# Optimization experiments

Hardware: AMD Instinct MI355X
Metric: run time of the kernel (lower is better)

Reference implementation:

```python
import jax, jax.numpy as jnp
import numpy as np

EPS = 1e-6
B, T, E, H = 2, 512, 1024, 256
NUM_BLOCK = 12


def normalize(x):
    # RMS-style normalization over the feature dim (no learned affine)
    return x * jax.lax.rsqrt(jnp.mean(x * x, axis=-1, keepdims=True) + EPS)


def bar_quadratic_causal(a, b):
    # y_i = (1/i) * sum_{j<=i} relu(a_i + b_j)   (causal prefix mean of pairwise relation)
    # a, b: [B, T, H]
    Tn = a.shape[1]
    pair = jax.nn.relu(a[:, :, None, :] + b[:, None, :, :])  # [B, T(i), T(j), H]
    mask = jnp.tril(jnp.ones((Tn, Tn), dtype=a.dtype))        # causal j<=i
    s = jnp.einsum('bijh,ij->bih', pair, mask)
    counts = jnp.arange(1, Tn + 1, dtype=a.dtype)[None, :, None]
    return s / counts


def setup_inputs() -> dict:
    key = jax.random.key(0)
    k0, k1, k2, k3 = jax.random.split(key, 4)
    x = jax.random.normal(k0, (B, T, E), dtype=jnp.float32)
    w1 = jax.random.normal(k1, (E, H), dtype=jnp.float32) * 0.02
    b1 = jnp.zeros((H,), dtype=jnp.float32)
    w2 = jax.random.normal(k2, (E, H), dtype=jnp.float32) * 0.02
    b2 = jnp.zeros((H,), dtype=jnp.float32)
    w3 = jax.random.normal(k3, (H, E), dtype=jnp.float32) * (0.02 / np.sqrt(NUM_BLOCK))
    b3 = jnp.zeros((E,), dtype=jnp.float32)
    return {"x": x, "w1": w1, "b1": b1, "w2": w2, "b2": b2, "w3": w3, "b3": b3}


def reference(x, w1, b1, w2, b2, w3, b3):
    r = normalize(x)
    a = r @ w1 + b1
    b = r @ w2 + b2
    # PreNorm == 'approx': normalize a and b separately
    a = normalize(a)
    b = normalize(b)
    r = bar_quadratic_causal(a, b)
    # PostNorm == 'yes'
    r = normalize(r)
    r = r @ w3 + b3
    return x + r
```

## Files before the change

kernel.cpp:

```cpp
#include <hip/hip_runtime.h>

#define EPSF 1e-6f
#define Bsz 2
#define Tn  512
#define En  1024
#define Hn  256
#define Mtot (Bsz * Tn)
typedef unsigned short us_t;
typedef unsigned int   u32_t;

typedef __attribute__((ext_vector_type(8))) __fp16 f16x8;
typedef __attribute__((ext_vector_type(2))) __fp16 h2_t;
typedef __attribute__((ext_vector_type(8))) short  short8;
typedef __attribute__((ext_vector_type(4))) float  f32x4;
#define MFMA16(a, b, c) __builtin_amdgcn_mfma_f32_16x16x32_f16((a), (b), (c), 0, 0, 0)

__device__ __forceinline__ us_t f2h(float f) {
  __fp16 h = (__fp16)f;
  return __builtin_bit_cast(us_t, h);
}
__device__ __forceinline__ float h2f(us_t u) {
  return (float)__builtin_bit_cast(__fp16, u);
}
__device__ __forceinline__ uint2 pack4h(float a, float b, float c, float d) {
  uint2 r;
  r.x = (u32_t)f2h(a) | ((u32_t)f2h(b) << 16);
  r.y = (u32_t)f2h(c) | ((u32_t)f2h(d) << 16);
  return r;
}
__device__ __forceinline__ float block_reduce_sum_256(float v, float* smem) {
  #pragma unroll
  for (int off = 32; off > 0; off >>= 1) v += __shfl_down(v, off, 64);
  const int wave = threadIdx.x >> 6;
  if ((threadIdx.x & 63) == 0) smem[wave] = v;
  __syncthreads();
  float s = smem[0] + smem[1] + smem[2] + smem[3];
  __syncthreads();
  return s;
}

__global__ __launch_bounds__(256) void k_prep(
    const float* __restrict__ x,
    const float* __restrict__ w1, const float* __restrict__ w2,
    const float* __restrict__ w3,
    us_t* __restrict__ xb, float* __restrict__ rs,
    us_t* __restrict__ w1t, us_t* __restrict__ w2t, us_t* __restrict__ w3t)
{
  const int b = blockIdx.x, t = threadIdx.x;

  if (b < 256) {
    const int wid = t >> 6, lane = t & 63;
    const int q   = b >> 3;
    const int mt  = (b & 7) + 8 * (q & 7);
    const int row = 16 * mt + 4 * (q >> 3) + wid;
    const float4* xp = (const float4*)(x + (size_t)row * En);
    float4 v[4];
    #pragma unroll
    for (int i = 0; i < 4; ++i) v[i] = xp[lane + 64 * i];
    float ss = 0.f;
    #pragma unroll
    for (int i = 0; i < 4; ++i)
      ss += v[i].x*v[i].x + v[i].y*v[i].y + v[i].z*v[i].z + v[i].w*v[i].w;
    #pragma unroll
    for (int off = 32; off > 0; off >>= 1) ss += __shfl_xor(ss, off, 64);
    if (lane == 0) rs[row] = rsqrtf(ss * (1.0f / En) + EPSF);
    uint2* xo = (uint2*)(xb + (size_t)row * En);
    #pragma unroll
    for (int i = 0; i < 4; ++i)
      xo[lane + 64 * i] = pack4h(v[i].x, v[i].y, v[i].z, v[i].w);
    return;
  }

  __shared__ float ts[32][33];
  const int i = b - 256;
  const float* src; us_t* dst; int R, C, tr, tc;
  if (i < 256)      { src = w1; dst = w1t; R = 1024; C = 256;  tr = i >> 3;  tc = i & 7; }
  else if (i < 512) { int k = i - 256; src = w2; dst = w2t; R = 1024; C = 256; tr = k >> 3; tc = k & 7; }
  else              { int k = i - 512; src = w3; dst = w3t; R = 256; C = 1024; tr = k >> 5; tc = k & 31; }

  const int r = t >> 3, c4 = (t & 7) * 4;
  float4 v = *(const float4*)(src + (size_t)(tr * 32 + r) * C + tc * 32 + c4);
  ts[r][c4 + 0] = v.x; ts[r][c4 + 1] = v.y; ts[r][c4 + 2] = v.z; ts[r][c4 + 3] = v.w;
  __syncthreads();
  float o0 = ts[c4 + 0][r], o1 = ts[c4 + 1][r], o2 = ts[c4 + 2][r], o3 = ts[c4 + 3][r];
  *(uint2*)(dst + (size_t)(tc * 32 + r) * R + tr * 32 + c4) = pack4h(o0, o1, o2, o3);
}

__global__ __launch_bounds__(256, 4) void k_gemm(
    const us_t* __restrict__ xb,
    const us_t* __restrict__ w1t, const us_t* __restrict__ w2t,
    float* __restrict__ Praw)
{
  const int blk = blockIdx.x;
  const int mt = blk & 63, nt = blk >> 6;
  const int m0 = mt * 16, n0 = nt * 32;
  const int wid = threadIdx.x >> 6, lane = threadIdx.x & 63;
  const int lg = lane >> 4, lr = lane & 15;
  const int k0 = wid * 256;

  const us_t* ap = xb + (size_t)(m0 + lr) * En + k0 + lg * 8;
  const us_t* bbase = (n0 < Hn) ? (w1t + (size_t)n0 * En)
                                : (w2t + (size_t)(n0 - Hn) * En);
  const us_t* bp0 = bbase + (size_t)lr * En + k0 + lg * 8;
  const us_t* bp1 = bp0 + (size_t)16 * En;

  f16x8 a[8], wf0[8], wf1[8];
  #pragma unroll
  for (int s = 0; s < 8; ++s) a[s]   = *(const f16x8*)(ap  + s * 32);
  #pragma unroll
  for (int s = 0; s < 8; ++s) wf0[s] = *(const f16x8*)(bp0 + s * 32);
  #pragma unroll
  for (int s = 0; s < 8; ++s) wf1[s] = *(const f16x8*)(bp1 + s * 32);

  f32x4 acc0 = {0.f,0.f,0.f,0.f}, acc1 = acc0;
  #pragma unroll
  for (int s = 0; s < 8; ++s) {
    acc0 = MFMA16(a[s], wf0[s], acc0);
    acc1 = MFMA16(a[s], wf1[s], acc1);
  }

  __shared__ float cmb[4][16][32];
  #pragma unroll
  for (int i = 0; i < 4; ++i) {
    cmb[wid][lg * 4 + i][lr]      = acc0[i];
    cmb[wid][lg * 4 + i][16 + lr] = acc1[i];
  }
  __syncthreads();

  #pragma unroll
  for (int e = 0; e < 2; ++e) {
    const int idx = threadIdx.x + e * 256;
    const int row = idx >> 5, col = idx & 31;
    float s = cmb[0][row][col] + cmb[1][row][col]
            + cmb[2][row][col] + cmb[3][row][col];
    Praw[(size_t)(m0 + row) * 512 + n0 + col] = s;
  }
}

__global__ __launch_bounds__(256) void k_norm(
    const float* __restrict__ Praw, const float* __restrict__ rs,
    const float* __restrict__ b2, us_t* __restrict__ BmT)
{
  const int blk = blockIdx.x, t = threadIdx.x;
  const int wid = t >> 6, lane = t & 63;
  const int h0 = lane * 4;

  __shared__ us_t ls[4][256];
  const int mt = blk & 63, sub = blk >> 6;
  const int r0 = 16 * mt + 4 * sub;
  const int r  = r0 + wid;

  float4 d = *(const float4*)(Praw + (size_t)r * 512 + Hn + h0);
  const float s0 = rs[r];
  float4 bv = *(const float4*)(b2 + h0);
  float vx = d.x * s0 + bv.x, vy = d.y * s0 + bv.y;
  float vz = d.z * s0 + bv.z, vw = d.w * s0 + bv.w;

  float ss = vx*vx + vy*vy + vz*vz + vw*vw;
  #pragma unroll
  for (int o2 = 32; o2 > 0; o2 >>= 1) ss += __shfl_xor(ss, o2, 64);
  const float sc = rsqrtf(ss * (1.0f / Hn) + EPSF);

  *(uint2*)&ls[wid][h0] = pack4h(vx*sc, vy*sc, vz*sc, vw*sc);
  __syncthreads();

  const int h = t;
  u32_t w0  = (u32_t)ls[0][h] | ((u32_t)ls[1][h] << 16);
  u32_t w1v = (u32_t)ls[2][h] | ((u32_t)ls[3][h] << 16);
  const int bb   = r0 >> 9;
  const int tcol = r0 & 511;
  *(uint2*)(BmT + (size_t)bb * Hn * Tn + (size_t)h * Tn + tcol) = make_uint2(w0, w1v);
}

#define JCHB 32
__global__ __launch_bounds__(256) void k_bar(
    const float* __restrict__ Praw, const float* __restrict__ rs,
    const float* __restrict__ b1,
    const us_t* __restrict__ BmT, us_t* __restrict__ Yb)
{
  __shared__ float red[4];
  const int raw = blockIdx.x;
  const int sel = (raw < 256) ? raw : (511 - raw);
  const int bb  = raw >> 8;
  const int i0  = sel * 2;
  const int h   = threadIdx.x;
  const int rg  = bb * Tn + i0;
  const size_t baseY = (size_t)bb * Tn * Hn;
  const us_t* __restrict__ bt = BmT + (size_t)bb * Hn * Tn + (size_t)h * Tn;

  const float b1h = b1[h];
  float v0 = fmaf(Praw[(size_t)rg * 512 + h],       rs[rg],     b1h);
  float v1 = fmaf(Praw[(size_t)(rg + 1) * 512 + h], rs[rg + 1], b1h);
  float ss0 = block_reduce_sum_256(v0 * v0, red);
  float ss1 = block_reduce_sum_256(v1 * v1, red);
  const float av0 = v0 * rsqrtf(ss0 * (1.0f / Hn) + EPSF);
  const float av1 = v1 * rsqrtf(ss1 * (1.0f / Hn) + EPSF);

  const __fp16 a0h = (__fp16)av0;
  const __fp16 a1h = (__fp16)av1;
  h2_t z2;  z2[0]  = (__fp16)0.f; z2[1]  = (__fp16)0.f;
  h2_t a02; a02[0] = a0h;         a02[1] = a0h;
  h2_t a12; a12[0] = a1h;         a12[1] = a1h;
  float sum0 = 0.f, sum1 = 0.f;

  const int nfull = i0 & ~(JCHB - 1);
  short8 c0[4], c1[4];

  #define LOADC(dst, jj) { _Pragma("unroll") \
    for (int q = 0; q < 4; ++q) dst[q] = *(const short8*)(bt + (jj) + q * 8); }
  #define PROCP(buf) { _Pragma("unroll") \
    for (int q = 0; q < 4; ++q) { \
      const h2_t* ph = (const h2_t*)&buf[q]; \
      h2_t p0 = z2, p1 = z2; \
      _Pragma("unroll") \
      for (int w2i = 0; w2i < 4; ++w2i) { \
        h2_t bv2 = ph[w2i]; \
        p0 += __builtin_elementwise_max(a02 + bv2, z2); \
        p1 += __builtin_elementwise_max(a12 + bv2, z2); \
      } \
      sum0 += (float)p0[0] + (float)p0[1]; \
      sum1 += (float)p1[0] + (float)p1[1]; } }

  if (nfull > 0) {
    LOADC(c0, 0);
    int j = 0;
    while (true) {
      const bool m1 = (j + JCHB     < nfull);
      const bool m2 = (j + 2 * JCHB < nfull);
      if (m1) LOADC(c1, j + JCHB);
      PROCP(c0);
      j += JCHB;
      if (!m1) break;
      if (m2) LOADC(c0, j + JCHB);
      PROCP(c1);
      j += JCHB;
      if (!m2) break;
    }
  }
  {
    short8 ct[4];
    LOADC(ct, nfull);
    const int lim = i0 - nfull;
    #pragma unroll
    for (int q = 0; q < 4; ++q)
      #pragma unroll
      for (int e = 0; e < 8; ++e) {
        const int jl = q * 8 + e;
        float bv = h2f((us_t)ct[q][e]);
        sum0 += (jl <= lim)     ? fmaxf((float)a0h + bv, 0.f) : 0.f;
        sum1 += (jl <= lim + 1) ? fmaxf((float)a1h + bv, 0.f) : 0.f;
      }
  }
  #undef LOADC
  #undef PROCP

  {
    float ss = block_reduce_sum_256(sum0 * sum0, red);
    float c  = (float)(i0 + 1);
    float sc = rsqrtf(ss * (1.0f / Hn) + EPSF * c * c);
    Yb[baseY + (size_t)i0 * Hn + h] = f2h(sum0 * sc);
  }
  {
    float ss = block_reduce_sum_256(sum1 * sum1, red);
    float c  = (float)(i0 + 2);
    float sc = rsqrtf(ss * (1.0f / Hn) + EPSF * c * c);
    Yb[baseY + (size_t)(i0 + 1) * Hn + h] = f2h(sum1 * sc);
  }
}

__global__ __launch_bounds__(256, 4) void k_out(
    const us_t* __restrict__ Yb, const us_t* __restrict__ w3t,
    const float* __restrict__ x, const float* __restrict__ b3,
    float* __restrict__ out)
{
  const int wid = threadIdx.x >> 6, lane = threadIdx.x & 63;
  const int wg = blockIdx.x * 4 + wid;
  const int nt = wg & 63, mt = wg >> 6;
  const int m0 = mt * 16, n0 = nt * 16;
  const int lg = lane >> 4, lr = lane & 15;

  const us_t* ap = Yb  + (size_t)(m0 + lr) * Hn + lg * 8;
  const us_t* bp = w3t + (size_t)(n0 + lr) * Hn + lg * 8;

  f16x8 a[8], b[8];
  #pragma unroll
  for (int s = 0; s < 8; ++s) a[s] = *(const f16x8*)(ap + s * 32);
  #pragma unroll
  for (int s = 0; s < 8; ++s) b[s] = *(const f16x8*)(bp + s * 32);

  f32x4 acc = {0.f,0.f,0.f,0.f};
  #pragma unroll
  for (int s = 0; s < 8; ++s) acc = MFMA16(a[s], b[s], acc);

  const int row = m0 + lg * 4;
  const int c = n0 + lr;
  const float bv = b3[c];
  #pragma unroll
  for (int i = 0; i < 4; ++i) {
    const size_t o = (size_t)(row + i) * En + c;
    out[o] = x[o] + acc[i] + bv;
  }
}

extern "C" void kernel_launch(void* const* d_in, const int* in_sizes, int n_in,
                              void* d_out, int out_size, void* d_ws, size_t ws_size,
                              hipStream_t stream) {
  const float* x  = (const float*)d_in[0];
  const float* w1 = (const float*)d_in[1];
  const float* b1 = (const float*)d_in[2];
  const float* w2 = (const float*)d_in[3];
  const float* b2 = (const float*)d_in[4];
  const float* w3 = (const float*)d_in[5];
  const float* b3 = (const float*)d_in[6];
  float* out = (float*)d_out;

  char* q = (char*)d_ws;
  float* Praw = (float*)q;  q += (size_t)Mtot * 512 * 4;
  us_t* xb    = (us_t*)q;   q += (size_t)Mtot * En * 2;
  us_t* w1t   = (us_t*)q;   q += (size_t)Hn * En * 2;
  us_t* w2t   = (us_t*)q;   q += (size_t)Hn * En * 2;
  us_t* w3t   = (us_t*)q;   q += (size_t)En * Hn * 2;
  us_t* BmT   = (us_t*)q;   q += (size_t)Mtot * Hn * 2;
  us_t* Yb    = (us_t*)q;   q += (size_t)Mtot * Hn * 2;
  float* rs   = (float*)q;  q += (size_t)Mtot * 4;

  k_prep<<<1024, 256, 0, stream>>>(x, w1, w2, w3, xb, rs, w1t, w2t, w3t);
  k_gemm<<<1024, 256, 0, stream>>>(xb, w1t, w2t, Praw);
  k_norm<<<256,  256, 0, stream>>>(Praw, rs, b2, BmT);
  k_bar <<<512,  256, 0, stream>>>(Praw, rs, b1, BmT, Yb);
  k_out <<<1024, 256, 0, stream>>>(Yb, w3t, x, b3, out);
}
```

Baseline: 47.06 us.

## Stage GEMM weight tiles through LDS via direct global-to-LDS loads

The projection GEMM now copies each wave's weight slice into swizzled shared memory with global_load_lds, instead of loading it into registers with per-lane vector loads. Each block now computes a 16-wide N tile rather than 32 wide, and the grid grows from 1024 to 2048 blocks. The aim is more coalesced weight fetches, lower register pressure and more parallelism. In exchange, the activation rows are loaded twice as often, and each block adds an extra barrier plus LDS round trips.

```diff
diff --git a/kernel.cpp b/kernel.cpp
--- a/kernel.cpp
+++ b/kernel.cpp
@@ -15,6 +15,10 @@
 typedef __attribute__((ext_vector_type(4))) float  f32x4;
 #define MFMA16(a, b, c) __builtin_amdgcn_mfma_f32_16x16x32_f16((a), (b), (c), 0, 0, 0)
 
+#define GLOAD_LDS16(g, l) __builtin_amdgcn_global_load_lds( \
+  (const __attribute__((address_space(1))) unsigned int*)(g), \
+  (__attribute__((address_space(3))) unsigned int*)(l), 16, 0, 0)
+
 __device__ __forceinline__ us_t f2h(float f) {
   __fp16 h = (__fp16)f;
   return __builtin_bit_cast(us_t, h);
@@ -91,50 +95,51 @@
     const us_t* __restrict__ w1t, const us_t* __restrict__ w2t,
     float* __restrict__ Praw)
 {
+  __shared__ us_t Bs[4][16][256];
+  __shared__ float cmb[4][16][16];
+
   const int blk = blockIdx.x;
   const int mt = blk & 63, nt = blk >> 6;
-  const int m0 = mt * 16, n0 = nt * 32;
-  const int wid = threadIdx.x >> 6, lane = threadIdx.x & 63;
+  const int m0 = mt * 16, n0 = nt * 16;
+  const int t = threadIdx.x;
+  const int wid = t >> 6, lane = t & 63;
   const int lg = lane >> 4, lr = lane & 15;
   const int k0 = wid * 256;
 
   const us_t* ap = xb + (size_t)(m0 + lr) * En + k0 + lg * 8;
+  f16x8 a[8];
+  #pragma unroll
+  for (int s = 0; s < 8; ++s) a[s] = *(const f16x8*)(ap + s * 32);
+
   const us_t* bbase = (n0 < Hn) ? (w1t + (size_t)n0 * En)
                                 : (w2t + (size_t)(n0 - Hn) * En);
-  const us_t* bp0 = bbase + (size_t)lr * En + k0 + lg * 8;
-  const us_t* bp1 = bp0 + (size_t)16 * En;
-
-  f16x8 a[8], wf0[8], wf1[8];
-  #pragma unroll
-  for (int s = 0; s < 8; ++s) a[s]   = *(const f16x8*)(ap  + s * 32);
-  #pragma unroll
-  for (int s = 0; s < 8; ++s) wf0[s] = *(const f16x8*)(bp0 + s * 32);
-  #pragma unroll
-  for (int s = 0; s < 8; ++s) wf1[s] = *(const f16x8*)(bp1 + s * 32);
-
-  f32x4 acc0 = {0.f,0.f,0.f,0.f}, acc1 = acc0;
+  #pragma unroll
+  for (int i = 0; i < 8; ++i) {
+    const int r   = 2 * i + (lane >> 5);
+    const int c2b = ((lane & 31) * 16) ^ ((r & 7) << 4);
+    const us_t* g = bbase + (size_t)r * En + k0 + (c2b >> 1);
+    GLOAD_LDS16(g, &Bs[wid][2 * i][0]);
+  }
+  __syncthreads();
+
+  f32x4 acc = {0.f,0.f,0.f,0.f};
+  const us_t* bs = &Bs[wid][0][0];
   #pragma unroll
   for (int s = 0; s < 8; ++s) {
-    acc0 = MFMA16(a[s], wf0[s], acc0);
-    acc1 = MFMA16(a[s], wf1[s], acc1);
-  }
-
-  __shared__ float cmb[4][16][32];
-  #pragma unroll
-  for (int i = 0; i < 4; ++i) {
-    cmb[wid][lg * 4 + i][lr]      = acc0[i];
-    cmb[wid][lg * 4 + i][16 + lr] = acc1[i];
-  }
-  __syncthreads();
-
-  #pragma unroll
-  for (int e = 0; e < 2; ++e) {
-    const int idx = threadIdx.x + e * 256;
-    const int row = idx >> 5, col = idx & 31;
-    float s = cmb[0][row][col] + cmb[1][row][col]
-            + cmb[2][row][col] + cmb[3][row][col];
-    Praw[(size_t)(m0 + row) * 512 + n0 + col] = s;
-  }
+    const int c2 = (lg * 16 + s * 64) ^ ((lr & 7) << 4);
+    f16x8 b = *(const f16x8*)(bs + lr * 256 + (c2 >> 1));
+    acc = MFMA16(a[s], b, acc);
+  }
+
+  #pragma unroll
+  for (int i = 0; i < 4; ++i)
+    cmb[wid][lg * 4 + i][lr] = acc[i];
+  __syncthreads();
+
+  const int row = t >> 4, col = t & 15;
+  float s2 = cmb[0][row][col] + cmb[1][row][col]
+           + cmb[2][row][col] + cmb[3][row][col];
+  Praw[(size_t)(m0 + row) * 512 + n0 + col] = s2;
 }
 
 __global__ __launch_bounds__(256) void k_norm(
@@ -325,7 +330,7 @@
   float* rs   = (float*)q;  q += (size_t)Mtot * 4;
 
   k_prep<<<1024, 256, 0, stream>>>(x, w1, w2, w3, xb, rs, w1t, w2t, w3t);
-  k_gemm<<<1024, 256, 0, stream>>>(xb, w1t, w2t, Praw);
+  k_gemm<<<2048, 256, 0, stream>>>(xb, w1t, w2t, Praw);
   k_norm<<<256,  256, 0, stream>>>(Praw, rs, b2, BmT);
   k_bar <<<512,  256, 0, stream>>>(Praw, rs, b1, BmT, Yb);
   k_out <<<1024, 256, 0, stream>>>(Yb, w3t, x, b3, out);
```

Result: no change. 46.57 us (-1.0%).
